# Kernel optimization log

Hardware: AMD Instinct MI355X
Metric: run time of the kernel (lower is better)

The kernel has to match this reference:

```python
import jax, jax.numpy as jnp
import numpy as np

N = 200000   # total nodes across batch
E = 800000   # total edges (avg degree 4)
G = 64       # number of graphs in batch
NGT = 30     # num gate types
EMB = 64     # gate_type_embed_dim
H = 128      # h_feats
INTER = 128  # inter_dim
EPS = 1e-12  # F.normalize eps


def _xavier(key, shape):
    fan_in, fan_out = shape
    std = np.sqrt(2.0 / (fan_in + fan_out))
    return jax.random.normal(key, shape, dtype=jnp.float32) * std


def setup_inputs() -> dict:
    key = jax.random.key(0)
    ks = jax.random.split(key, 12)
    gate_type = jax.random.randint(ks[0], (N,), 0, NGT)
    src = jax.random.randint(ks[1], (E,), 0, N)
    dst = jax.random.randint(ks[2], (E,), 0, N)
    w = jax.random.uniform(ks[3], (E, 3), dtype=jnp.float32)
    node2graph = (jnp.arange(N) * G) // N  # sorted segment ids, even split
    emb = jax.random.normal(ks[4], (NGT, EMB), dtype=jnp.float32)
    return {
        "gate_type": gate_type, "src": src, "dst": dst, "w": w,
        "node2graph": node2graph, "emb": emb,
        "W1_0": _xavier(ks[5], (EMB + 3, INTER)), "b1_0": jnp.zeros((INTER,), jnp.float32),
        "W2_0": _xavier(ks[6], (EMB + INTER, H)),
        "W1_1": _xavier(ks[7], (H + 3, INTER)), "b1_1": jnp.zeros((INTER,), jnp.float32),
        "W2_1": _xavier(ks[8], (H + INTER, H)),
        "W1_2": _xavier(ks[9], (H + 3, INTER)), "b1_2": jnp.zeros((INTER,), jnp.float32),
        "W2_2": _xavier(ks[10], (H + INTER, H)),
    }


def _qconv(h, src, dst, w, W1, b1, W2):
    # message: cat(h[src], w) per edge; linear1+ReLU per message; sum per dst node
    m = jnp.concatenate([h[src], w], axis=1)          # [E, in+3]
    t = jax.nn.relu(m @ W1 + b1)                      # [E, inter]
    h_N = jax.ops.segment_sum(t, dst, num_segments=h.shape[0])  # [N, inter]
    h_lin = jax.nn.relu(jnp.concatenate([h, h_N], axis=1) @ W2)  # [N, out]
    norm = jnp.linalg.norm(h_lin, axis=-1, keepdims=True)
    return h_lin / jnp.maximum(norm, EPS)             # F.normalize(p=2, dim=-1)


def reference(gate_type, src, dst, w, node2graph, emb,
              W1_0, b1_0, W2_0, W1_1, b1_1, W2_1, W1_2, b1_2, W2_2):
    h = emb[gate_type]                                # [N, EMB]
    layers = [(W1_0, b1_0, W2_0), (W1_1, b1_1, W2_1), (W1_2, b1_2, W2_2)]
    readouts = []
    for W1, b1, W2 in layers:
        h = _qconv(h, src, dst, w, W1, b1, W2)
        readouts.append(jax.ops.segment_sum(h, node2graph, num_segments=G))  # [G, H]
    return h, jnp.concatenate(readouts, axis=1)       # [N,H], [G, 3H]
```

## Files before the change

### kernel.cpp

```cpp
#include <hip/hip_runtime.h>
#include <hip/hip_bf16.h>
#include <hip/hip_fp16.h>

typedef _Float16 half8 __attribute__((ext_vector_type(8)));
typedef _Float16 half4 __attribute__((ext_vector_type(4)));
typedef _Float16 h2    __attribute__((ext_vector_type(2)));
typedef float floatx4 __attribute__((ext_vector_type(4)));

__device__ __forceinline__ _Float16 f2h(float f) { return (_Float16)f; }


__global__ void fill_dummy_kernel(int4* __restrict__ eData, int cap, int N, int NGT)
{
    int i = blockIdx.x * 256 + threadIdx.x;
    if (i < cap) { int4 v = {N | (NGT << 24), N, 0, 0}; eData[i] = v; }
}

__global__ void hist_kernel(const int* __restrict__ dst, int* __restrict__ cnt, int E)
{
    int e = blockIdx.x * 256 + threadIdx.x;
    if (e < E) atomicAdd(&cnt[dst[e]], 1);
}

__global__ void scan1p_kernel(const int* __restrict__ cnt, int* __restrict__ offP,
                              int n, int* __restrict__ blockSums)
{
    __shared__ int sm[256];
    const int t = threadIdx.x;
    const int base = blockIdx.x * 1024 + t * 4;
    int v[4]; int s = 0;
#pragma unroll
    for (int i = 0; i < 4; ++i) {
        v[i] = (base + i < n) ? ((cnt[base + i] + 3) & ~3) : 0;
        s += v[i];
    }
    sm[t] = s; __syncthreads();
#pragma unroll
    for (int off = 1; off < 256; off <<= 1) {
        int y = (t >= off) ? sm[t - off] : 0;
        __syncthreads();
        if (t >= off) sm[t] += y;
        __syncthreads();
    }
    int excl = sm[t] - s;
    if (t == 255) blockSums[blockIdx.x] = sm[255];
    int run = excl;
#pragma unroll
    for (int i = 0; i < 4; ++i) {
        if (base + i < n) offP[base + i] = run;
        run += v[i];
    }
}

__global__ void scan2_kernel(int* __restrict__ blockSums, int nb)
{
    __shared__ int sm[256];
    const int t = threadIdx.x;
    int s = (t < nb) ? blockSums[t] : 0;
    sm[t] = s; __syncthreads();
#pragma unroll
    for (int off = 1; off < 256; off <<= 1) {
        int y = (t >= off) ? sm[t - off] : 0;
        __syncthreads();
        if (t >= off) sm[t] += y;
        __syncthreads();
    }
    if (t < nb) blockSums[t] = sm[t] - s;
}

__global__ void scan3_kernel(int* __restrict__ offP, int n, const int* __restrict__ blockSums)
{
    const int base = blockIdx.x * 1024 + threadIdx.x * 4;
    const int add = blockSums[blockIdx.x];
#pragma unroll
    for (int i = 0; i < 4; ++i)
        if (base + i < n) offP[base + i] += add;
}

__global__ void scatter_kernel(const int* __restrict__ src, const int* __restrict__ dst,
                               const float* __restrict__ w, const int* __restrict__ gt,
                               const int* __restrict__ offP, int* __restrict__ cur,
                               int4* __restrict__ eData, int E)
{
    int e = blockIdx.x * 256 + threadIdx.x;
    if (e >= E) return;
    int d = dst[e];
    int p = offP[d] + atomicAdd(&cur[d], 1);
    int s = src[e];
    h2 w01 = { f2h(w[(size_t)e * 3 + 0]), f2h(w[(size_t)e * 3 + 1]) };
    h2 w2o = { f2h(w[(size_t)e * 3 + 2]), (_Float16)1.0f };
    int4 v = { s | (gt[s] << 24), d,
               __builtin_bit_cast(int, w01), __builtin_bit_cast(int, w2o) };
    eData[p] = v;
}

__global__ void ginfo_kernel(const int4* __restrict__ eData, unsigned* __restrict__ gInfo,
                             int nGroups, int N)
{
    int g = blockIdx.x * 256 + threadIdx.x;
    if (g >= nGroups) return;
    const int* ei = (const int*)eData;
    int d = ei[16 * g + 1];
    if (d >= N) { gInfo[g] = 0xFFFFFFFFu; return; }
    bool multi = (g > 0 && ei[16 * (g - 1) + 1] == d) || (ei[16 * (g + 1) + 1] == d);
    gInfo[g] = (unsigned)d | (multi ? 0x80000000u : 0u);
}

__global__ void wprep_kernel(const float* __restrict__ W, _Float16* __restrict__ out,
                             int K, int KP)
{
    int idx = blockIdx.x * 256 + threadIdx.x;
    if (idx >= 128 * KP) return;
    int f = idx / KP, k = idx % KP;
    float v = (k < K) ? W[(size_t)k * 128 + f] : 0.0f;
    out[idx] = f2h(v);
}

__global__ void wwprep_kernel(const float* __restrict__ W1, int rowOff,
                              _Float16* __restrict__ out)
{
    int idx = blockIdx.x * 256 + threadIdx.x;
    if (idx < 3 * 128) out[idx] = f2h(W1[(size_t)(rowOff + idx / 128) * 128 + (idx & 127)]);
}

__global__ void embW1_kernel(const float* __restrict__ emb, const float* __restrict__ W1,
                             const float* __restrict__ b1, _Float16* __restrict__ out, int NGT)
{
    int idx = blockIdx.x * 256 + threadIdx.x;
    if (idx >= (NGT + 1) * 128) return;
    int g = idx >> 7, f = idx & 127;
    float s = 0.0f;
    if (g < NGT) {
        s = b1[f];
        for (int k = 0; k < 64; ++k) s += emb[g * 64 + k] * W1[(size_t)k * 128 + f];
    }
    out[idx] = f2h(s);
}

__global__ void embW2_kernel(const float* __restrict__ emb, const float* __restrict__ W2,
                             float* __restrict__ out, int NGT)
{
    int idx = blockIdx.x * 256 + threadIdx.x;
    if (idx >= NGT * 128) return;
    int g = idx >> 7, f = idx & 127;
    float s = 0.0f;
    for (int k = 0; k < 64; ++k) s += emb[g * 64 + k] * W2[(size_t)k * 128 + f];
    out[idx] = s;
}

__global__ void __launch_bounds__(512, 2)
hw1_kernel(const _Float16* __restrict__ hA,
           const _Float16* __restrict__ WT,
           const float* __restrict__ b1,
           _Float16* __restrict__ out,
           int N, int tilesPerWave, int nTiles)
{
    __shared__ __align__(16) _Float16 lds[128 * 128];
    const int tid = threadIdx.x;
    for (int s = tid; s < 128 * 16; s += 512) {
        const int row = s / 16, seg = s % 16;
        half8 v = *(const half8*)(WT + (size_t)row * 128 + seg * 8);
        *(half8*)(&lds[row * 128 + ((seg ^ (row & 7)) * 8)]) = v;
    }
    __syncthreads();

    const int lane = tid & 63;
    const int wv   = tid >> 6;
    const int lRow = lane & 15;
    const int lGrp = lane >> 4;

    float b1v[8];
#pragma unroll
    for (int jt = 0; jt < 8; ++jt) b1v[jt] = b1[jt * 16 + lRow];

    const int wave = blockIdx.x * 8 + wv;
    const int t0 = wave * tilesPerWave;
    const int t1 = min(t0 + tilesPerWave, nTiles);

    for (int tile = t0; tile < t1; ++tile) {
        const int i0 = tile * 16;
        const int iA = min(i0 + lRow, N - 1);
        half8 a[4];
#pragma unroll
        for (int kc = 0; kc < 4; ++kc)
            a[kc] = *(const half8*)(hA + (size_t)iA * 128 + kc * 32 + lGrp * 8);

        floatx4 acc[8] = {};
#pragma unroll
        for (int jt = 0; jt < 8; ++jt) {
            const int row = jt * 16 + lRow;
            const int sw = row & 7;
#pragma unroll
            for (int kc = 0; kc < 4; ++kc) {
                half8 b = *(const half8*)(&lds[row * 128 + (((kc * 4 + lGrp) ^ sw) * 8)]);
                acc[jt] = __builtin_amdgcn_mfma_f32_16x16x32_f16(a[kc], b, acc[jt], 0, 0, 0);
            }
        }
#pragma unroll
        for (int r = 0; r < 4; ++r) {
            const int i = i0 + lGrp * 4 + r;
            if (i < N) {
#pragma unroll
                for (int jt = 0; jt < 8; ++jt)
                    out[(size_t)i * 128 + jt * 16 + lRow] = f2h(acc[jt][r] + b1v[jt]);
            }
        }
    }
}

template<bool L0, bool H16>
__global__ void __launch_bounds__(256, 8)
edgeW_kernel(const _Float16* __restrict__ T,
             const _Float16* __restrict__ Wwh,
             const int4* __restrict__ eData,
             const unsigned* __restrict__ gInfo,
             void* __restrict__ hNv, int groupsPerWave, int nGroups)
{
    const int tid  = threadIdx.x;
    const int lane = tid & 63;
    const int wv   = tid >> 6;
    const int sub  = lane >> 5;
    const int col4 = (lane & 31) * 4;

    const h2 z = {(_Float16)0.0f, (_Float16)0.0f};
    const h2 w0a = *(const h2*)(Wwh + 0 * 128 + col4);
    const h2 w0b = *(const h2*)(Wwh + 0 * 128 + col4 + 2);
    const h2 w1a = *(const h2*)(Wwh + 1 * 128 + col4);
    const h2 w1b = *(const h2*)(Wwh + 1 * 128 + col4 + 2);
    const h2 w2a = *(const h2*)(Wwh + 2 * 128 + col4);
    const h2 w2b = *(const h2*)(Wwh + 2 * 128 + col4 + 2);

    const int wave = blockIdx.x * 4 + wv;
    const int g0 = wave * groupsPerWave;
    const int g1 = min(g0 + groupsPerWave, nGroups);

    auto doGroup = [&](int g) {
        const unsigned gi = gInfo[g];
        if (gi == 0xFFFFFFFFu) return;
        const int dG = (int)(gi & 0xFFFFFFu);
        const bool multi = (gi >> 31) != 0;
        const int eb = g * 4;
        const int4 ea = eData[eb + sub];
        const int4 eb2 = eData[eb + 2 + sub];
        const int ra = L0 ? (ea.x >> 24) : (ea.x & 0xFFFFFF);
        const int rb = L0 ? (eb2.x >> 24) : (eb2.x & 0xFFFFFF);
        const h2 wa01 = __builtin_bit_cast(h2, ea.z);
        const h2 wa2o = __builtin_bit_cast(h2, ea.w);
        const h2 wb01 = __builtin_bit_cast(h2, eb2.z);
        const h2 wb2o = __builtin_bit_cast(h2, eb2.w);
        const half4 Tav = *(const half4*)(T + (size_t)ra * 128 + col4);
        const half4 Tbv = *(const half4*)(T + (size_t)rb * 128 + col4);
        const h2 Ta0 = {Tav[0], Tav[1]}, Ta1 = {Tav[2], Tav[3]};
        const h2 Tb0 = {Tbv[0], Tbv[1]}, Tb1 = {Tbv[2], Tbv[3]};

        h2 ma0 = Ta0 + wa01[0] * w0a + wa01[1] * w1a + wa2o[0] * w2a;
        h2 ma1 = Ta1 + wa01[0] * w0b + wa01[1] * w1b + wa2o[0] * w2b;
        h2 mb0 = Tb0 + wb01[0] * w0a + wb01[1] * w1a + wb2o[0] * w2a;
        h2 mb1 = Tb1 + wb01[0] * w0b + wb01[1] * w1b + wb2o[0] * w2b;
        h2 r0 = __builtin_elementwise_max(ma0, z) + __builtin_elementwise_max(mb0, z);
        h2 r1 = __builtin_elementwise_max(ma1, z) + __builtin_elementwise_max(mb1, z);
        int o0 = __shfl_xor(__builtin_bit_cast(int, r0), 32);
        int o1 = __shfl_xor(__builtin_bit_cast(int, r1), 32);
        r0 = r0 + __builtin_bit_cast(h2, o0);
        r1 = r1 + __builtin_bit_cast(h2, o1);

        if (lane < 32) {
            if (H16) {
                if (multi) {
                    __half2* a0p = (__half2*)((__half*)hNv + (size_t)dG * 128 + col4);
                    unsafeAtomicAdd(a0p, __builtin_bit_cast(__half2, r0));
                    unsafeAtomicAdd(a0p + 1, __builtin_bit_cast(__half2, r1));
                } else {
                    int2 pk = { __builtin_bit_cast(int, r0), __builtin_bit_cast(int, r1) };
                    *(int2*)((__half*)hNv + (size_t)dG * 128 + col4) = pk;
                }
            } else {
                float f0 = (float)r0[0], f1 = (float)r0[1];
                float f2 = (float)r1[0], f3 = (float)r1[1];
                float* a0p = (float*)hNv + (size_t)dG * 128 + col4;
                if (multi) {
                    unsafeAtomicAdd(a0p + 0, f0); unsafeAtomicAdd(a0p + 1, f1);
                    unsafeAtomicAdd(a0p + 2, f2); unsafeAtomicAdd(a0p + 3, f3);
                } else {
                    floatx4 p = {f0, f1, f2, f3};
                    *(floatx4*)a0p = p;
                }
            }
        }
    };

    int g = g0;
    for (; g + 1 < g1; g += 2) { doGroup(g); doGroup(g + 1); }
    if (g < g1) doGroup(g);
}

template<bool H16, bool L0, bool LAST>
__global__ void __launch_bounds__(256, 2)
node_kernel(const _Float16* __restrict__ hA,
            const void* __restrict__ hNv,
            const _Float16* __restrict__ W2T,
            const float* __restrict__ embW2,
            const int* __restrict__ gt,
            const int* __restrict__ n2g,
            _Float16* __restrict__ hOut,
            float* __restrict__ fOut,
            float* __restrict__ readout,
            int N, int tilesPerWave, int nTiles, int layerOff)
{
    constexpr int K2  = L0 ? 128 : 256;
    constexpr int KCA = L0 ? 0 : 4;
    constexpr int KC  = K2 / 32;
    constexpr int SPR = K2 / 8;
    __shared__ __align__(16) _Float16 lds[128 * K2];

    const int tid = threadIdx.x;
    for (int s = tid; s < 128 * SPR; s += 256) {
        const int row = s / SPR, seg = s % SPR;
        half8 v = *(const half8*)(W2T + (size_t)row * K2 + seg * 8);
        *(half8*)(&lds[row * K2 + ((seg ^ (row & 7)) * 8)]) = v;
    }
    __syncthreads();

    const int lane = tid & 63;
    const int wv   = tid >> 6;
    const int lRow = lane & 15;
    const int lGrp = lane >> 4;
    const int wave = blockIdx.x * 4 + wv;
    const int t0 = wave * tilesPerWave;
    const int t1 = min(t0 + tilesPerWave, nTiles);
    if (t0 >= t1) return;

    int gCur = -1; float racc[8];
#pragma unroll
    for (int jt = 0; jt < 8; ++jt) racc[jt] = 0.0f;

    auto loadA = [&](int i0, half8 (&afrag)[KC]) {
        const int iA = min(i0 + lRow, N - 1);
#pragma unroll
        for (int kc = 0; kc < KCA; ++kc)
            afrag[kc] = *(const half8*)(hA + (size_t)iA * 128 + kc * 32 + lGrp * 8);
        if (H16) {
            const _Float16* hN = (const _Float16*)hNv;
#pragma unroll
            for (int kc = KCA; kc < KC; ++kc)
                afrag[kc] = *(const half8*)(hN + (size_t)iA * 128 + (kc - KCA) * 32 + lGrp * 8);
        } else {
            const float* hN = (const float*)hNv;
#pragma unroll
            for (int kc = KCA; kc < KC; ++kc) {
                const float* p = hN + (size_t)iA * 128 + (kc - KCA) * 32 + lGrp * 8;
                floatx4 f0 = *(const floatx4*)(p);
                floatx4 f1 = *(const floatx4*)(p + 4);
                half8 a;
#pragma unroll
                for (int i = 0; i < 4; ++i) { a[i] = f2h(f0[i]); a[i + 4] = f2h(f1[i]); }
                afrag[kc] = a;
            }
        }
    };

    auto epilogue = [&](int i0, floatx4 (&acc)[8]) {
        if (L0) {
#pragma unroll
            for (int r = 0; r < 4; ++r) {
                const int i = min(i0 + lGrp * 4 + r, N - 1);
                const int g_t = gt[i];
#pragma unroll
                for (int jt = 0; jt < 8; ++jt)
                    acc[jt][r] += embW2[(size_t)g_t * 128 + jt * 16 + lRow];
            }
        }
        float scl[4];
#pragma unroll
        for (int r = 0; r < 4; ++r) {
            float s = 0.f;
#pragma unroll
            for (int jt = 0; jt < 8; ++jt) {
                float v = fmaxf(acc[jt][r], 0.0f);
                s += v * v;
            }
#pragma unroll
            for (int m = 1; m <= 8; m <<= 1) s += __shfl_xor(s, m);
            scl[r] = 1.0f / fmaxf(sqrtf(s), 1e-12f);
        }
#pragma unroll
        for (int r = 0; r < 4; ++r) {
            const int i = i0 + lGrp * 4 + r;
            if (i < N) {
#pragma unroll
                for (int jt = 0; jt < 8; ++jt) {
                    float v = fmaxf(acc[jt][r], 0.0f) * scl[r];
                    if (LAST) fOut[(size_t)i * 128 + jt * 16 + lRow] = v;
                    else      hOut[(size_t)i * 128 + jt * 16 + lRow] = f2h(v);
                }
            }
        }
        const int gFirst = n2g[min(i0, N - 1)];
        const int gLast  = n2g[min(i0 + 15, N - 1)];
        if (gFirst == gLast && i0 + 15 < N) {
            if (gFirst != gCur) {
                if (gCur >= 0 && lane < 16) {
#pragma unroll
                    for (int jt = 0; jt < 8; ++jt)
                        unsafeAtomicAdd(&readout[(size_t)gCur * 384 + layerOff + jt * 16 + lane], racc[jt]);
                }
                gCur = gFirst;
#pragma unroll
                for (int jt = 0; jt < 8; ++jt) racc[jt] = 0.0f;
            }
#pragma unroll
            for (int jt = 0; jt < 8; ++jt) {
                float t = 0.f;
#pragma unroll
                for (int r = 0; r < 4; ++r) t += fmaxf(acc[jt][r], 0.0f) * scl[r];
                t += __shfl_xor(t, 16);
                t += __shfl_xor(t, 32);
                racc[jt] += t;
            }
        } else {
            if (gCur >= 0 && lane < 16) {
#pragma unroll
                for (int jt = 0; jt < 8; ++jt)
                    unsafeAtomicAdd(&readout[(size_t)gCur * 384 + layerOff + jt * 16 + lane], racc[jt]);
            }
            gCur = -1;
#pragma unroll
            for (int jt = 0; jt < 8; ++jt) racc[jt] = 0.0f;
#pragma unroll
            for (int r = 0; r < 4; ++r) {
                const int i = i0 + lGrp * 4 + r;
                if (i < N) {
                    const int g = n2g[i];
#pragma unroll
                    for (int jt = 0; jt < 8; ++jt) {
                        float v = fmaxf(acc[jt][r], 0.0f) * scl[r];
                        unsafeAtomicAdd(&readout[(size_t)g * 384 + layerOff + jt * 16 + lRow], v);
                    }
                }
            }
        }
    };

    for (int tile = t0; tile < t1; tile += 2) {
        const bool has2 = (tile + 1 < t1);
        const int i0a = tile * 16;
        const int i0b = has2 ? (tile + 1) * 16 : i0a;

        half8 afA[KC], afB[KC];
        loadA(i0a, afA);
        loadA(i0b, afB);

        floatx4 accA[8] = {}, accB[8] = {};
#pragma unroll
        for (int jt = 0; jt < 8; ++jt) {
            const int rb = (jt * 16 + lRow) * K2;
            const int sw = (jt * 16 + lRow) & 7;
#pragma unroll
            for (int kc = 0; kc < KC; ++kc) {
                half8 b = *(const half8*)(&lds[rb + (((kc * 4 + lGrp) ^ sw) * 8)]);
                accA[jt] = __builtin_amdgcn_mfma_f32_16x16x32_f16(afA[kc], b, accA[jt], 0, 0, 0);
                accB[jt] = __builtin_amdgcn_mfma_f32_16x16x32_f16(afB[kc], b, accB[jt], 0, 0, 0);
            }
        }
        epilogue(i0a, accA);
        if (has2) epilogue(i0b, accB);
    }
    if (gCur >= 0 && lane < 16) {
#pragma unroll
        for (int jt = 0; jt < 8; ++jt)
            unsafeAtomicAdd(&readout[(size_t)gCur * 384 + layerOff + jt * 16 + lane], racc[jt]);
    }
}

extern "C" void kernel_launch(void* const* d_in, const int* in_sizes, int n_in,
                              void* d_out, int out_size, void* d_ws, size_t ws_size,
                              hipStream_t stream)
{
    const int*   gate_type = (const int*)d_in[0];
    const int*   src  = (const int*)d_in[1];
    const int*   dst  = (const int*)d_in[2];
    const float* wE   = (const float*)d_in[3];
    const int*   n2g  = (const int*)d_in[4];
    const float* emb  = (const float*)d_in[5];
    const float* W1_0 = (const float*)d_in[6];
    const float* b1_0 = (const float*)d_in[7];
    const float* W2_0 = (const float*)d_in[8];
    const float* W1_1 = (const float*)d_in[9];
    const float* b1_1 = (const float*)d_in[10];
    const float* W2_1 = (const float*)d_in[11];
    const float* W1_2 = (const float*)d_in[12];
    const float* b1_2 = (const float*)d_in[13];
    const float* W2_2 = (const float*)d_in[14];

    const int N = in_sizes[0];
    const int E = in_sizes[1];
    const int NGT = in_sizes[5] / 64;
    const int cap = (E + 3 * N + 15) & ~15;

    char* ws = (char*)d_ws;
    size_t off = 0;
    auto alloc = [&](size_t bytes) { void* p = ws + off; off = (off + bytes + 255) & ~255ULL; return p; };
    _Float16* hBuf  = (_Float16*)alloc((size_t)N * 128 * 2);
    int4*     eData = (int4*)alloc(((size_t)cap + 16) * 16);
    unsigned* gInfo = (unsigned*)alloc(((size_t)cap / 4 + 4) * 4);
    int*      cnt   = (int*)alloc((size_t)N * 4);
    int*      offP  = (int*)alloc((size_t)N * 4);
    int*      cur   = (int*)alloc((size_t)N * 4);
    int*      bSums = (int*)alloc(256 * 4);
    _Float16* W1T1  = (_Float16*)alloc((size_t)128 * 128 * 2);
    _Float16* W1T2  = (_Float16*)alloc((size_t)128 * 128 * 2);
    _Float16* W2T0  = (_Float16*)alloc((size_t)128 * 128 * 2);
    _Float16* W2T1  = (_Float16*)alloc((size_t)128 * 256 * 2);
    _Float16* W2T2  = (_Float16*)alloc((size_t)128 * 256 * 2);
    _Float16* Wwh0  = (_Float16*)alloc((size_t)3 * 128 * 2);
    _Float16* Wwh1  = (_Float16*)alloc((size_t)3 * 128 * 2);
    _Float16* Wwh2  = (_Float16*)alloc((size_t)3 * 128 * 2);
    _Float16* eW1b  = (_Float16*)alloc((size_t)(NGT + 1) * 128 * 2);
    float*    eW2   = (float*)alloc((size_t)NGT * 128 * 4);
    _Float16* hW1b  = (_Float16*)alloc(((size_t)N + 1) * 128 * 2);
    size_t hn16_off = off;
    const bool h16 = (ws_size >= hn16_off + (size_t)N * 128 * 2 + 256);
    _Float16* hN16 = (_Float16*)alloc((size_t)N * 128 * 2);

    float* readout = (float*)d_out + (size_t)N * 128;
    void*  hN      = h16 ? (void*)hN16 : (void*)d_out;

    const int nGroups = cap / 4;
    const int nTiles  = (N + 15) / 16;
    const int EB = 2048;
    const int gpw = (nGroups + EB * 4 - 1) / (EB * 4);
    const int NB = 512;
    const int tpwN = (nTiles + NB * 4 - 1) / (NB * 4);
    const int HB = 256;
    const int tpwH = (nTiles + HB * 8 - 1) / (HB * 8);
    const int nb = (N + 1023) / 1024;

    hipMemsetAsync(cnt, 0, (size_t)N * 4, stream);
    hipMemsetAsync(cur, 0, (size_t)N * 4, stream);
    hipMemsetAsync(hW1b + (size_t)N * 128, 0, 256, stream);
    fill_dummy_kernel<<<(cap + 16 + 255) / 256, 256, 0, stream>>>(eData, cap + 16, N, NGT);
    hist_kernel<<<(E + 255) / 256, 256, 0, stream>>>(dst, cnt, E);
    scan1p_kernel<<<nb, 256, 0, stream>>>(cnt, offP, N, bSums);
    scan2_kernel<<<1, 256, 0, stream>>>(bSums, nb);
    scan3_kernel<<<nb, 256, 0, stream>>>(offP, N, bSums);
    scatter_kernel<<<(E + 255) / 256, 256, 0, stream>>>(src, dst, wE, gate_type,
                                                        offP, cur, eData, E);
    ginfo_kernel<<<(nGroups + 255) / 256, 256, 0, stream>>>(eData, gInfo, nGroups, N);

    embW1_kernel<<<((NGT + 1) * 128 + 255) / 256, 256, 0, stream>>>(emb, W1_0, b1_0, eW1b, NGT);
    embW2_kernel<<<(NGT * 128 + 255) / 256, 256, 0, stream>>>(emb, W2_0, eW2, NGT);
    wprep_kernel<<<(128 * 128 + 255) / 256, 256, 0, stream>>>(W1_1, W1T1, 128, 128);
    wprep_kernel<<<(128 * 128 + 255) / 256, 256, 0, stream>>>(W1_2, W1T2, 128, 128);
    wprep_kernel<<<(128 * 128 + 255) / 256, 256, 0, stream>>>(W2_0 + (size_t)64 * 128, W2T0, 128, 128);
    wprep_kernel<<<(128 * 256 + 255) / 256, 256, 0, stream>>>(W2_1, W2T1, 256, 256);
    wprep_kernel<<<(128 * 256 + 255) / 256, 256, 0, stream>>>(W2_2, W2T2, 256, 256);
    wwprep_kernel<<<2, 256, 0, stream>>>(W1_0, 64, Wwh0);
    wwprep_kernel<<<2, 256, 0, stream>>>(W1_1, 128, Wwh1);
    wwprep_kernel<<<2, 256, 0, stream>>>(W1_2, 128, Wwh2);

    if (h16) {
        hipMemsetAsync(readout, 0, (size_t)(out_size - N * 128) * 4, stream);
        hipMemsetAsync(hN16, 0, (size_t)N * 128 * 2, stream);
        edgeW_kernel<true, true><<<EB, 256, 0, stream>>>(eW1b, Wwh0, eData, gInfo, hN, gpw, nGroups);
        node_kernel<true, true, false><<<NB, 256, 0, stream>>>(nullptr, hN, W2T0, eW2, gate_type, n2g,
                                                               hBuf, nullptr, readout, N, tpwN, nTiles, 0);
        hw1_kernel<<<HB, 512, 0, stream>>>(hBuf, W1T1, b1_1, hW1b, N, tpwH, nTiles);
        hipMemsetAsync(hN16, 0, (size_t)N * 128 * 2, stream);
        edgeW_kernel<false, true><<<EB, 256, 0, stream>>>(hW1b, Wwh1, eData, gInfo, hN, gpw, nGroups);
        node_kernel<true, false, false><<<NB, 256, 0, stream>>>(hBuf, hN, W2T1, nullptr, nullptr, n2g,
                                                                hBuf, nullptr, readout, N, tpwN, nTiles, 128);
        hw1_kernel<<<HB, 512, 0, stream>>>(hBuf, W1T2, b1_2, hW1b, N, tpwH, nTiles);
        hipMemsetAsync(hN16, 0, (size_t)N * 128 * 2, stream);
        edgeW_kernel<false, true><<<EB, 256, 0, stream>>>(hW1b, Wwh2, eData, gInfo, hN, gpw, nGroups);
        node_kernel<true, false, true><<<NB, 256, 0, stream>>>(hBuf, hN, W2T2, nullptr, nullptr, n2g,
                                                               nullptr, (float*)d_out, readout, N, tpwN, nTiles, 256);
    } else {
        hipMemsetAsync(d_out, 0, (size_t)out_size * 4, stream);
        edgeW_kernel<true, false><<<EB, 256, 0, stream>>>(eW1b, Wwh0, eData, gInfo, hN, gpw, nGroups);
        node_kernel<false, true, false><<<NB, 256, 0, stream>>>(nullptr, hN, W2T0, eW2, gate_type, n2g,
                                                                hBuf, nullptr, readout, N, tpwN, nTiles, 0);
        hw1_kernel<<<HB, 512, 0, stream>>>(hBuf, W1T1, b1_1, hW1b, N, tpwH, nTiles);
        hipMemsetAsync(d_out, 0, (size_t)N * 128 * 4, stream);
        edgeW_kernel<false, false><<<EB, 256, 0, stream>>>(hW1b, Wwh1, eData, gInfo, hN, gpw, nGroups);
        node_kernel<false, false, false><<<NB, 256, 0, stream>>>(hBuf, hN, W2T1, nullptr, nullptr, n2g,
                                                                 hBuf, nullptr, readout, N, tpwN, nTiles, 128);
        hw1_kernel<<<HB, 512, 0, stream>>>(hBuf, W1T2, b1_2, hW1b, N, tpwH, nTiles);
        hipMemsetAsync(d_out, 0, (size_t)N * 128 * 4, stream);
        edgeW_kernel<false, false><<<EB, 256, 0, stream>>>(hW1b, Wwh2, eData, gInfo, hN, gpw, nGroups);
        node_kernel<false, false, true><<<NB, 256, 0, stream>>>(hBuf, hN, W2T2, nullptr, nullptr, n2g,
                                                                nullptr, (float*)d_out, readout, N, tpwN, nTiles, 256);
    }
}
```

Before: 589.6 us.

## Accumulate per-destination runs in registers, atomics only across wave boundaries

The edge kernel now walks its contiguous groups, accumulates the messages of consecutive groups that share a destination node in registers, and flushes once per run. Atomics are used only when a node's groups span more than one wave's range, which ginfo computes from the CSR offsets and the groups-per-wave value. This cuts atomic traffic and redundant partial writes for high-degree nodes. It also drops the 2x manual unroll, and the launch-bounds occupancy hint goes from 8 to 4 blocks, which may change register allocation.

```diff
diff --git a/kernel.cpp b/kernel.cpp
--- a/kernel.cpp
+++ b/kernel.cpp
@@ -94,16 +94,21 @@
     eData[p] = v;
 }
 
-__global__ void ginfo_kernel(const int4* __restrict__ eData, unsigned* __restrict__ gInfo,
-                             int nGroups, int N)
+__global__ void ginfo_kernel(const int4* __restrict__ eData,
+                             const int* __restrict__ cnt, const int* __restrict__ offP,
+                             unsigned* __restrict__ gInfo,
+                             int nGroups, int N, int gpw)
 {
     int g = blockIdx.x * 256 + threadIdx.x;
     if (g >= nGroups) return;
     const int* ei = (const int*)eData;
     int d = ei[16 * g + 1];
     if (d >= N) { gInfo[g] = 0xFFFFFFFFu; return; }
-    bool multi = (g > 0 && ei[16 * (g - 1) + 1] == d) || (ei[16 * (g + 1) + 1] == d);
-    gInfo[g] = (unsigned)d | (multi ? 0x80000000u : 0u);
+    int cntP = (cnt[d] + 3) & ~3;
+    int gA = offP[d] >> 2;
+    int gB = gA + (cntP >> 2) - 1;
+    bool cross = (gA / gpw) != (gB / gpw);
+    gInfo[g] = (unsigned)d | (cross ? 0x80000000u : 0u);
 }
 
 __global__ void wprep_kernel(const float* __restrict__ W, _Float16* __restrict__ out,
@@ -209,7 +214,7 @@
 }
 
 template<bool L0, bool H16>
-__global__ void __launch_bounds__(256, 8)
+__global__ void __launch_bounds__(256, 4)
 edgeW_kernel(const _Float16* __restrict__ T,
              const _Float16* __restrict__ Wwh,
              const int4* __restrict__ eData,
@@ -233,21 +238,55 @@
     const int wave = blockIdx.x * 4 + wv;
     const int g0 = wave * groupsPerWave;
     const int g1 = min(g0 + groupsPerWave, nGroups);
-
-    auto doGroup = [&](int g) {
+    if (g0 >= g1) return;
+
+    int runD = -1; bool runCross = false;
+    h2 a0 = z, a1 = z;
+
+    auto flush = [&]() {
+        if (runD < 0) return;
+        h2 s0 = a0, s1 = a1;
+        int o0 = __shfl_xor(__builtin_bit_cast(int, s0), 32);
+        int o1 = __shfl_xor(__builtin_bit_cast(int, s1), 32);
+        s0 = s0 + __builtin_bit_cast(h2, o0);
+        s1 = s1 + __builtin_bit_cast(h2, o1);
+        if (lane < 32) {
+            if (H16) {
+                if (runCross) {
+                    __half2* a0p = (__half2*)((__half*)hNv + (size_t)runD * 128 + col4);
+                    unsafeAtomicAdd(a0p, __builtin_bit_cast(__half2, s0));
+                    unsafeAtomicAdd(a0p + 1, __builtin_bit_cast(__half2, s1));
+                } else {
+                    int2 pk = { __builtin_bit_cast(int, s0), __builtin_bit_cast(int, s1) };
+                    *(int2*)((__half*)hNv + (size_t)runD * 128 + col4) = pk;
+                }
+            } else {
+                float f0 = (float)s0[0], f1 = (float)s0[1];
+                float f2 = (float)s1[0], f3 = (float)s1[1];
+                float* a0p = (float*)hNv + (size_t)runD * 128 + col4;
+                if (runCross) {
+                    unsafeAtomicAdd(a0p + 0, f0); unsafeAtomicAdd(a0p + 1, f1);
+                    unsafeAtomicAdd(a0p + 2, f2); unsafeAtomicAdd(a0p + 3, f3);
+                } else {
+                    floatx4 p = {f0, f1, f2, f3};
+                    *(floatx4*)a0p = p;
+                }
+            }
+        }
+    };
+
+    for (int g = g0; g < g1; ++g) {
         const unsigned gi = gInfo[g];
-        if (gi == 0xFFFFFFFFu) return;
+        if (gi == 0xFFFFFFFFu) break;
         const int dG = (int)(gi & 0xFFFFFFu);
-        const bool multi = (gi >> 31) != 0;
-        const int eb = g * 4;
-        const int4 ea = eData[eb + sub];
-        const int4 eb2 = eData[eb + 2 + sub];
+        const int4 ea = eData[g * 4 + sub];
+        const int4 eb = eData[g * 4 + 2 + sub];
         const int ra = L0 ? (ea.x >> 24) : (ea.x & 0xFFFFFF);
-        const int rb = L0 ? (eb2.x >> 24) : (eb2.x & 0xFFFFFF);
+        const int rb = L0 ? (eb.x >> 24) : (eb.x & 0xFFFFFF);
         const h2 wa01 = __builtin_bit_cast(h2, ea.z);
         const h2 wa2o = __builtin_bit_cast(h2, ea.w);
-        const h2 wb01 = __builtin_bit_cast(h2, eb2.z);
-        const h2 wb2o = __builtin_bit_cast(h2, eb2.w);
+        const h2 wb01 = __builtin_bit_cast(h2, eb.z);
+        const h2 wb2o = __builtin_bit_cast(h2, eb.w);
         const half4 Tav = *(const half4*)(T + (size_t)ra * 128 + col4);
         const half4 Tbv = *(const half4*)(T + (size_t)rb * 128 + col4);
         const h2 Ta0 = {Tav[0], Tav[1]}, Ta1 = {Tav[2], Tav[3]};
@@ -259,39 +298,16 @@
         h2 mb1 = Tb1 + wb01[0] * w0b + wb01[1] * w1b + wb2o[0] * w2b;
         h2 r0 = __builtin_elementwise_max(ma0, z) + __builtin_elementwise_max(mb0, z);
         h2 r1 = __builtin_elementwise_max(ma1, z) + __builtin_elementwise_max(mb1, z);
-        int o0 = __shfl_xor(__builtin_bit_cast(int, r0), 32);
-        int o1 = __shfl_xor(__builtin_bit_cast(int, r1), 32);
-        r0 = r0 + __builtin_bit_cast(h2, o0);
-        r1 = r1 + __builtin_bit_cast(h2, o1);
-
-        if (lane < 32) {
-            if (H16) {
-                if (multi) {
-                    __half2* a0p = (__half2*)((__half*)hNv + (size_t)dG * 128 + col4);
-                    unsafeAtomicAdd(a0p, __builtin_bit_cast(__half2, r0));
-                    unsafeAtomicAdd(a0p + 1, __builtin_bit_cast(__half2, r1));
-                } else {
-                    int2 pk = { __builtin_bit_cast(int, r0), __builtin_bit_cast(int, r1) };
-                    *(int2*)((__half*)hNv + (size_t)dG * 128 + col4) = pk;
-                }
-            } else {
-                float f0 = (float)r0[0], f1 = (float)r0[1];
-                float f2 = (float)r1[0], f3 = (float)r1[1];
-                float* a0p = (float*)hNv + (size_t)dG * 128 + col4;
-                if (multi) {
-                    unsafeAtomicAdd(a0p + 0, f0); unsafeAtomicAdd(a0p + 1, f1);
-                    unsafeAtomicAdd(a0p + 2, f2); unsafeAtomicAdd(a0p + 3, f3);
-                } else {
-                    floatx4 p = {f0, f1, f2, f3};
-                    *(floatx4*)a0p = p;
-                }
-            }
-        }
-    };
-
-    int g = g0;
-    for (; g + 1 < g1; g += 2) { doGroup(g); doGroup(g + 1); }
-    if (g < g1) doGroup(g);
+
+        if (dG == runD) {
+            a0 = a0 + r0; a1 = a1 + r1;
+        } else {
+            flush();
+            runD = dG; runCross = (gi >> 31) != 0;
+            a0 = r0; a1 = r1;
+        }
+    }
+    flush();
 }
 
 template<bool H16, bool L0, bool LAST>
@@ -545,7 +561,8 @@
     scan3_kernel<<<nb, 256, 0, stream>>>(offP, N, bSums);
     scatter_kernel<<<(E + 255) / 256, 256, 0, stream>>>(src, dst, wE, gate_type,
                                                         offP, cur, eData, E);
-    ginfo_kernel<<<(nGroups + 255) / 256, 256, 0, stream>>>(eData, gInfo, nGroups, N);
+    ginfo_kernel<<<(nGroups + 255) / 256, 256, 0, stream>>>(eData, cnt, offP, gInfo,
+                                                            nGroups, N, gpw);
 
     embW1_kernel<<<((NGT + 1) * 128 + 255) / 256, 256, 0, stream>>>(emb, W1_0, b1_0, eW1b, NGT);
     embW2_kernel<<<(NGT * 128 + 255) / 256, 256, 0, stream>>>(emb, W2_0, eW2, NGT);
```

Measured after the change: 519.1 us. 12.0% less time.
